# Performance work log

Hardware: AMD Instinct MI355X
Metric: run time of the kernel (lower is better)

The kernel has to match this reference:

```python
import jax, jax.numpy as jnp
import numpy as np

NF, IN_NF, N_LAYERS = 64, 196, 3
B, H, W = 1, 256, 256
P3 = [(1, 1), (1, 1)]
P1 = [(0, 0), (0, 0)]


def conv2d(x, w, pad):
    return jax.lax.conv_general_dilated(x, w, (1, 1), pad,
                                        dimension_numbers=('NCHW', 'OIHW', 'NCHW'))


def prelu(x, a):
    return jnp.where(x >= 0, x, a[None, :, None, None] * x)


def warp(x, flow):
    # standard backward bilinear warp, zero padding outside the image
    Bx, C, Hx, Wx = x.shape
    yy, xx = jnp.meshgrid(jnp.arange(Hx, dtype=x.dtype),
                          jnp.arange(Wx, dtype=x.dtype), indexing='ij')
    px = xx[None] + flow[:, 0]  # (B,H,W)
    py = yy[None] + flow[:, 1]

    def sample(img, px, py):  # img (C,H,W); px,py (H,W)
        x0 = jnp.floor(px)
        y0 = jnp.floor(py)
        x1 = x0 + 1.0
        y1 = y0 + 1.0
        wx1 = px - x0
        wx0 = 1.0 - wx1
        wy1 = py - y0
        wy0 = 1.0 - wy1

        def gather(xi, yi):
            valid = (xi >= 0) & (xi <= Wx - 1) & (yi >= 0) & (yi <= Hx - 1)
            xc = jnp.clip(xi, 0, Wx - 1).astype(jnp.int32)
            yc = jnp.clip(yi, 0, Hx - 1).astype(jnp.int32)
            return img[:, yc, xc] * valid.astype(img.dtype)

        return (gather(x0, y0) * (wx0 * wy0) + gather(x1, y0) * (wx1 * wy0)
                + gather(x0, y1) * (wx0 * wy1) + gather(x1, y1) * (wx1 * wy1))

    return jax.vmap(sample)(x, px, py)


def setup_inputs() -> dict:
    key = jax.random.key(0)
    ks = jax.random.split(key, 11)
    s = 0.05
    return {
        'feat_0': jax.random.normal(ks[0], (B, 64, H, W), jnp.float32),
        'feat_1': jax.random.normal(ks[1], (B, 64, H, W), jnp.float32),
        'feat_dense': jax.random.normal(ks[2], (B, 64, H, W), jnp.float32),
        'flow': jax.random.normal(ks[3], (B, 4, H, W), jnp.float32),
        'space_mask': jax.random.uniform(ks[4], (B, 1, H, W), jnp.float32),
        'head_w': jax.random.normal(ks[5], (IN_NF, IN_NF, 3, 3), jnp.float32) * s,
        'head_a': jnp.full((IN_NF,), 0.25, jnp.float32),
        'conv_w': jax.random.normal(ks[6], (N_LAYERS, IN_NF, IN_NF, 3, 3), jnp.float32) * s,
        'conv_a': jnp.full((N_LAYERS, IN_NF), 0.25, jnp.float32),
        'last_w': jax.random.normal(ks[7], (4 + NF, IN_NF * (N_LAYERS + 1), 1, 1), jnp.float32) * s,
        'last_b': jax.random.normal(ks[8], (4 + NF,), jnp.float32) * s,
        'mask_w': jax.random.normal(ks[9], (2, NF, 3, 3), jnp.float32) * s,
        'mask_b': jax.random.normal(ks[10], (2,), jnp.float32) * s,
    }


def reference(feat_0, feat_1, feat_dense, flow, space_mask,
              head_w, head_a, conv_w, conv_a, last_w, last_b, mask_w, mask_b):
    f0 = warp(feat_0, flow[:, :2])
    f1 = warp(feat_1, flow[:, 2:4])
    x = jnp.concatenate([f0, f1, feat_dense, flow], axis=1)  # (B, in_nf, H, W)
    sm_up = jnp.repeat(jnp.repeat(space_mask, 2, axis=2), 2, axis=3)

    # head: conv3x3 -> PReLU, then mask (dense / use_sparsity=False path)
    x = prelu(conv2d(x, head_w, P3), head_a) * space_mask
    outs = [x]
    for i in range(N_LAYERS):
        x = conv2d(x, conv_w[i], P3) * space_mask
        x = prelu(x, conv_a[i])
        outs.append(x)
    x = conv2d(jnp.concatenate(outs, axis=1), last_w, P1) + last_b[None, :, None, None]

    smn = conv2d(x[:, 4:], mask_w, P3) + mask_b[None, :, None, None]

    Bx, Cx, Hx, Wx = x.shape
    x_up = jax.image.resize(x, (Bx, Cx, 2 * Hx, 2 * Wx), method='bilinear')
    smn_up = jax.image.resize(smn, (Bx, 2, 2 * Hx, 2 * Wx), method='bilinear')

    flow_out = x_up[:, :4]
    feat_t = x_up[:, 4:]
    # eval-mode mask (training=False): hard argmax between channel 0 and 1
    mask_next = (smn_up[:, :1] > smn_up[:, 1:2]).astype(x.dtype) * sm_up
    return flow_out, feat_t, mask_next
```

## Files before the change

kernel.cpp:

```cpp
#include <hip/hip_runtime.h>

typedef _Float16 f16;
typedef _Float16 f16x8 __attribute__((ext_vector_type(8)));
typedef _Float16 f16x4 __attribute__((ext_vector_type(4)));
typedef float    f32x4 __attribute__((ext_vector_type(4)));
typedef float    f32x16 __attribute__((ext_vector_type(16)));

#define MFMA16(a,b,c) __builtin_amdgcn_mfma_f32_16x16x32_f16(a,b,c,0,0,0)
#define MFMA32(a,b,c) __builtin_amdgcn_mfma_f32_32x32x16_f16(a,b,c,0,0,0)

#define AS1 __attribute__((address_space(1)))
#define AS3 __attribute__((address_space(3)))

#define NPIX 65536
#define PXS   8
#define KHS   2064
#define K16S  4128
#define HS    8256
#define CBS   16512
#define ROWH  115584
#define RBYTES 231168
#define SBUF  ((size_t)258*RBYTES)

#define PKSUB  7168
#define PK_CONV 903168
#define NMICRO 117

#define PKL_CB  5120
#define PKL_BI  35840
#define PK1_S   3072
#define PK1_BI  39936

#define ASTG 14336

__global__ void k_pack_conv(const float* __restrict__ head_w,
                            const float* __restrict__ conv_w,
                            f16* __restrict__ dst)
{
    int t = blockIdx.x*256 + threadIdx.x;
    int lane = t & 63; t >>= 6;
    int ob  = t % 7;  t /= 7;
    int sel = t & 1;  t >>= 1;
    int kx  = t % 3;  t /= 3;
    int k16 = t & 1;  t >>= 1;
    int cb  = t % 7;  t /= 7;
    int ky  = t % 3;  t /= 3;
    int li  = t;
    if (li >= 4) return;
    if (cb == 6 && k16 == 1) return;
    const float* W = (li == 0) ? head_w : (conv_w + (size_t)(li-1)*196*196*9);
    int oc  = ob*32 + (lane & 31);
    int ic0 = cb*32 + k16*16 + (lane >> 5)*8;
    int tap = ky*3 + kx;
    f16x8 v;
#pragma unroll
    for (int j = 0; j < 8; ++j) {
        int ic = ic0 + j;
        float x = 0.f;
        if (oc < 196 && ic < 196) x = W[((size_t)oc*196 + ic)*9 + tap];
        f16 h = (f16)x;
        v[j] = (sel == 0) ? h : (f16)(x - (float)h);
    }
    int pos = ky*39 + ((cb < 6) ? (cb*6 + k16*3 + kx) : (36 + kx));
    *(f16x8*)(dst + (size_t)li*PK_CONV + (size_t)pos*PKSUB
              + (size_t)(sel*7 + ob)*512 + (size_t)lane*8) = v;
}

__global__ void k_pack_last(const float* __restrict__ last_w, f16* __restrict__ dst)
{
    int t = blockIdx.x*256 + threadIdx.x;
    if (t >= 4*7*5*2*64) return;
    int lane = t & 63; t >>= 6;
    int sel  = t & 1;  t >>= 1;
    int ob   = t % 5;  t /= 5;
    int cb   = t % 7;  t /= 7;
    int bi   = t;
    int oc = ob*16 + (lane & 15);
    int k0 = cb*32 + (lane >> 4)*8;
    f16x8 v;
#pragma unroll
    for (int j = 0; j < 8; ++j) {
        int k = k0 + j;
        float x = 0.f;
        if (oc < 68 && k < 196) x = last_w[(size_t)oc*784 + bi*196 + k];
        f16 h = (f16)x;
        v[j] = (sel == 0) ? h : (f16)(x - (float)h);
    }
    *(f16x8*)(dst + (((size_t)((bi*7+cb)*5 + ob)*2 + sel)*64 + lane)*8) = v;
}

__global__ void k_pack_last32(const float* __restrict__ last_w, f16* __restrict__ dst)
{
    int t = blockIdx.x*256 + threadIdx.x;
    if (t >= 4*13*2*3*64) return;
    int lane = t & 63; t >>= 6;
    int ob   = t % 3;  t /= 3;
    int sel  = t & 1;  t >>= 1;
    int s    = t % 13; t /= 13;
    int bi   = t;
    int cb  = (s < 12) ? (s >> 1) : 6;
    int k16 = (s < 12) ? (s & 1)  : 0;
    int oc  = ob*32 + (lane & 31);
    int ic0 = cb*32 + k16*16 + (lane >> 5)*8;
    f16x8 v;
#pragma unroll
    for (int j = 0; j < 8; ++j) {
        int ic = ic0 + j;
        float x = 0.f;
        if (oc < 68 && ic < 196) x = last_w[(size_t)oc*784 + bi*196 + ic];
        f16 h = (f16)x;
        v[j] = (sel == 0) ? h : (f16)(x - (float)h);
    }
    *(f16x8*)(dst + (size_t)bi*PK1_BI + (size_t)s*PK1_S
              + (size_t)(sel*3 + ob)*512 + (size_t)lane*8) = v;
}

__global__ void k_zero_halo(f16* __restrict__ bufA, f16* __restrict__ bufB)
{
    int c = blockIdx.x*256 + threadIdx.x;
    int end = c & 1; c >>= 1;
    int kh  = c & 1; c >>= 1;
    int k16 = c & 1; c >>= 1;
    int h   = c & 1; c >>= 1;
    int cb  = c % 7; c /= 7;
    int row = c % 258; c /= 258;
    if (c >= 2) return;
    f16* base = (c == 0) ? bufA : bufB;
    f16* p = base + (size_t)row*ROWH + cb*CBS + h*HS + k16*K16S + kh*KHS + (end ? 257 : 0)*PXS;
    f16x8 z = {(f16)0,(f16)0,(f16)0,(f16)0,(f16)0,(f16)0,(f16)0,(f16)0};
    *(f16x8*)p = z;
}

struct Gath { int o00,o01,o10,o11; float w00,w01,w10,w11; };

__device__ inline Gath mk_gath(float pxf, float pyf)
{
    float x0 = floorf(pxf), y0 = floorf(pyf);
    float x1 = x0 + 1.f, y1 = y0 + 1.f;
    float wx1 = pxf - x0, wx0 = 1.f - wx1;
    float wy1 = pyf - y0, wy0 = 1.f - wy1;
    bool vx0 = (x0 >= 0.f) && (x0 <= 255.f);
    bool vx1 = (x1 >= 0.f) && (x1 <= 255.f);
    bool vy0 = (y0 >= 0.f) && (y0 <= 255.f);
    bool vy1 = (y1 >= 0.f) && (y1 <= 255.f);
    int ix0 = min(max((int)x0, 0), 255);
    int ix1 = min(max((int)x1, 0), 255);
    int iy0 = min(max((int)y0, 0), 255);
    int iy1 = min(max((int)y1, 0), 255);
    Gath g;
    g.o00 = iy0*256 + ix0; g.w00 = (vx0 && vy0) ? wx0*wy0 : 0.f;
    g.o01 = iy0*256 + ix1; g.w01 = (vx1 && vy0) ? wx1*wy0 : 0.f;
    g.o10 = iy1*256 + ix0; g.w10 = (vx0 && vy1) ? wx0*wy1 : 0.f;
    g.o11 = iy1*256 + ix1; g.w11 = (vx1 && vy1) ? wx1*wy1 : 0.f;
    return g;
}

__device__ inline void store4n(f16* __restrict__ rowb, int slot, int c0,
                               float a, float b, float c, float d)
{
    f16x4 hi, lo;
    f16 h;
    h = (f16)a; hi[0] = h; lo[0] = (f16)(a - (float)h);
    h = (f16)b; hi[1] = h; lo[1] = (f16)(b - (float)h);
    h = (f16)c; hi[2] = h; lo[2] = (f16)(c - (float)h);
    h = (f16)d; hi[3] = h; lo[3] = (f16)(d - (float)h);
    int cb = c0 >> 5, w32 = c0 & 31;
    f16* p = rowb + cb*CBS + (w32 >> 4)*K16S + ((w32 >> 3) & 1)*KHS
                 + (size_t)slot*PXS + (w32 & 7);
    *(f16x4*)p        = hi;
    *(f16x4*)(p + HS) = lo;
}

__global__ void k_warp_concat(const float* __restrict__ f0, const float* __restrict__ f1,
                              const float* __restrict__ fd, const float* __restrict__ flow,
                              f16* __restrict__ out)
{
    int px = blockIdx.x*256 + threadIdx.x;
    int row = px >> 8, col = px & 255;
    f16* rowb = out + (size_t)(row+1)*ROWH;
    int slot = col + 1;
    Gath g0 = mk_gath((float)col + flow[px],          (float)row + flow[NPIX   + px]);
    Gath g1 = mk_gath((float)col + flow[2*NPIX + px], (float)row + flow[3*NPIX + px]);
#pragma unroll
    for (int c = 0; c < 64; c += 4) {
        float v[4];
#pragma unroll
        for (int r = 0; r < 4; ++r) {
            const float* im = f0 + (size_t)(c+r)*NPIX;
            v[r] = g0.w00*im[g0.o00] + g0.w01*im[g0.o01] + g0.w10*im[g0.o10] + g0.w11*im[g0.o11];
        }
        store4n(rowb, slot, c, v[0], v[1], v[2], v[3]);
    }
#pragma unroll
    for (int c = 0; c < 64; c += 4) {
        float v[4];
#pragma unroll
        for (int r = 0; r < 4; ++r) {
            const float* im = f1 + (size_t)(c+r)*NPIX;
            v[r] = g1.w00*im[g1.o00] + g1.w01*im[g1.o01] + g1.w10*im[g1.o10] + g1.w11*im[g1.o11];
        }
        store4n(rowb, slot, 64 + c, v[0], v[1], v[2], v[3]);
    }
#pragma unroll
    for (int c = 0; c < 64; c += 4) {
        store4n(rowb, slot, 128 + c, fd[(size_t)(c+0)*NPIX + px], fd[(size_t)(c+1)*NPIX + px],
                                     fd[(size_t)(c+2)*NPIX + px], fd[(size_t)(c+3)*NPIX + px]);
    }
    store4n(rowb, slot, 192, flow[px], flow[NPIX+px], flow[2*NPIX+px], flow[3*NPIX+px]);
#pragma unroll
    for (int c = 196; c < 224; c += 4) store4n(rowb, slot, c, 0.f, 0.f, 0.f, 0.f);
}

__global__ __launch_bounds__(256, 2)
void k_conv32(const f16* __restrict__ in, f16* __restrict__ out,
              const f16* __restrict__ pack, const float* __restrict__ alpha,
              const float* __restrict__ mask, const f16* __restrict__ pk1,
              const float* __restrict__ bias1, float* __restrict__ accp, int bi1)
{
    __shared__ __align__(16) char As[2][ASTG];

    int bid = blockIdx.x;
    int wg  = (bid & 7)*64 + (bid >> 3);
    int row  = wg >> 1;
    int half = wg & 1;
    int tid  = threadIdx.x;
    int lane = tid & 63;
    int w    = tid >> 6;
    int pxt  = half*4 + w;
    int l31 = lane & 31, lk = lane >> 5;

    f32x16 acc[7];
#pragma unroll
    for (int o = 0; o < 7; ++o)
#pragma unroll
        for (int e = 0; e < 16; ++e) acc[o][e] = 0.f;
    f32x16 acc1[3];
#pragma unroll
    for (int o = 0; o < 3; ++o)
#pragma unroll
        for (int e = 0; e < 16; ++e) acc1[o][e] = 0.f;

    auto stage = [&](int b, const f16* src) {
        __builtin_amdgcn_global_load_lds(
            (const AS1 void*)(src + (size_t)tid*8),
            (AS3 void*)(&As[b][0] + tid*16), 16, 0, 0);
        __builtin_amdgcn_global_load_lds(
            (const AS1 void*)(src + (size_t)(tid+256)*8),
            (AS3 void*)(&As[b][0] + (tid+256)*16), 16, 0, 0);
        __builtin_amdgcn_global_load_lds(
            (const AS1 void*)(src + (size_t)(tid+512)*8),
            (AS3 void*)(&As[b][0] + (tid+512)*16), 16, 0, 0);
        if (tid < 128)
            __builtin_amdgcn_global_load_lds(
                (const AS1 void*)(src + (size_t)(tid+768)*8),
                (AS3 void*)(&As[b][0] + (tid+768)*16), 16, 0, 0);
    };

    auto lB = [&](const f16* bp, f16x8& H, f16x8& L) {
        H = *(const f16x8*)bp;
        L = *(const f16x8*)(bp + HS);
    };

    const f16* bcol = in + (size_t)lk*KHS + (size_t)(pxt*32 + l31)*PXS;

    f16x8 Bh0, Bl0, Bh1, Bl1;
    stage(0, pack);
    lB(bcol + (size_t)row*ROWH, Bh0, Bl0);
    __syncthreads();

    int bsel = 0, q = 0;
    for (int ky = 0; ky < 3; ++ky) {
        const f16* brow = bcol + (size_t)(row + ky)*ROWH;
        for (int cb = 0; cb < 7; ++cb) {
            const f16* bcb = brow + cb*CBS;
            const f16* bnext = (cb < 6) ? (bcb + CBS) : (brow + ROWH);
            int nk16 = (cb == 6) ? 1 : 2;
            for (int k16 = 0; k16 < 2; ++k16) {
                if (k16 >= nk16) break;
#pragma unroll
                for (int kx = 0; kx < 3; ++kx) {
                    bool last = (q == NMICRO - 1);
                    if (!last) {
                        stage(bsel ^ 1, pack + (size_t)(q+1)*PKSUB);
                        const f16* nb;
                        if (kx < 2)                  nb = bcb + k16*K16S + (kx+1)*PXS;
                        else if (k16 == 0 && cb < 6) nb = bcb + K16S;
                        else                         nb = bnext;
                        lB(nb, Bh1, Bl1);
                    }
                    bool ctr = (ky == 1) && (kx == 1) && (bi1 >= 0);
                    f16x8 A1h[3], A1l[3];
                    if (ctr) {
                        int s = (cb < 6) ? (cb*2 + k16) : 12;
                        const f16* a1 = pk1 + (size_t)bi1*PK1_BI + (size_t)s*PK1_S
                                      + (size_t)lane*8;
#pragma unroll
                        for (int o = 0; o < 3; ++o) {
                            A1h[o] = *(const f16x8*)(a1 + o*512);
                            A1l[o] = *(const f16x8*)(a1 + (3+o)*512);
                        }
                    }
                    const char* ab = &As[bsel][0];
                    __builtin_amdgcn_s_setprio(1);
#pragma unroll
                    for (int o = 0; o < 7; ++o) {
                        f16x8 Ah = *(const f16x8*)(ab + o*1024 + lane*16);
                        f16x8 Al = *(const f16x8*)(ab + (7+o)*1024 + lane*16);
                        acc[o] = MFMA32(Ah, Bh0, acc[o]);
                        acc[o] = MFMA32(Al, Bh0, acc[o]);
                        acc[o] = MFMA32(Ah, Bl0, acc[o]);
                    }
                    if (ctr) {
#pragma unroll
                        for (int o = 0; o < 3; ++o) {
                            acc1[o] = MFMA32(A1h[o], Bh0, acc1[o]);
                            acc1[o] = MFMA32(A1l[o], Bh0, acc1[o]);
                            acc1[o] = MFMA32(A1h[o], Bl0, acc1[o]);
                        }
                    }
                    __builtin_amdgcn_s_setprio(0);
                    __syncthreads();
                    bsel ^= 1; ++q;
                    Bh0 = Bh1; Bl0 = Bl1;
                }
            }
        }
    }

    float mv = mask[row*256 + pxt*32 + l31];
    f16* orow = out + (size_t)(row+1)*ROWH + (size_t)(pxt*32 + l31 + 1)*PXS + lk*4;
#pragma unroll
    for (int o = 0; o < 7; ++o) {
#pragma unroll
        for (int qg = 0; qg < 4; ++qg) {
            int oc0 = o*32 + 8*qg + 4*lk;
            f32x4 a4 = *(const f32x4*)(alpha + min(oc0, 192));
            f16x4 hi, lo;
#pragma unroll
            for (int e = 0; e < 4; ++e) {
                float v = acc[o][qg*4 + e];
                v = (v >= 0.f ? v : a4[e]*v) * mv;
                f16 h = (f16)v;
                hi[e] = h;
                lo[e] = (f16)(v - (float)h);
            }
            f16* p = orow + o*CBS + (qg >> 1)*K16S + (qg & 1)*KHS;
            *(f16x4*)p        = hi;
            *(f16x4*)(p + HS) = lo;
        }
    }
    if (bi1 >= 0) {
        int px = row*256 + pxt*32 + l31;
        float* dst = accp + (size_t)px*72;
#pragma unroll
        for (int o = 0; o < 3; ++o) {
#pragma unroll
            for (int qg = 0; qg < 4; ++qg) {
                int oc0 = o*32 + 8*qg + 4*lk;
                if (oc0 >= 72) continue;
                f32x4 d;
#pragma unroll
                for (int e = 0; e < 4; ++e) d[e] = acc1[o][qg*4 + e];
                if (bi1 == 0) {
                    f32x4 b4;
#pragma unroll
                    for (int e = 0; e < 4; ++e) b4[e] = bias1[min(oc0 + e, 67)];
                    *(f32x4*)(dst + oc0) = d + b4;
                } else {
                    *(f32x4*)(dst + oc0) = *(const f32x4*)(dst + oc0) + d;
                }
            }
        }
    }
}

__global__ __launch_bounds__(256, 4)
void k_acc_last(const f16* __restrict__ in, const f16* __restrict__ pack,
                const float* __restrict__ bias, float* __restrict__ accp, int bi)
{
    int lane = threadIdx.x & 63;
    int wid  = (blockIdx.x << 2) | (threadIdx.x >> 6);
    int row  = wid >> 3;
    int col0 = (wid & 7) << 5;
    int l15 = lane & 15, lk = lane >> 4;

    f32x4 acc[5][2];
#pragma unroll
    for (int i = 0; i < 5; ++i)
#pragma unroll
        for (int j = 0; j < 2; ++j)
            acc[i][j] = (f32x4){0.f, 0.f, 0.f, 0.f};

    const f16* bb = in + (size_t)(row+1)*ROWH + (size_t)(col0 + l15 + 1)*PXS
                  + (lk >> 1)*K16S + (lk & 1)*KHS;
    const f16* ap = pack + (size_t)bi*PKL_BI + (size_t)lane*8;
    for (int cb = 0; cb < 7; ++cb) {
        f16x8 bh[2], bl[2];
#pragma unroll
        for (int pb = 0; pb < 2; ++pb) {
            const f16* p = bb + cb*CBS + pb*16*PXS;
            bh[pb] = *(const f16x8*)p;
            bl[pb] = *(const f16x8*)(p + HS);
        }
        const f16* a = ap + cb*PKL_CB;
#pragma unroll
        for (int ob = 0; ob < 5; ++ob) {
            f16x8 ah = *(const f16x8*)(a + ob*1024);
            f16x8 al = *(const f16x8*)(a + ob*1024 + 512);
#pragma unroll
            for (int pb = 0; pb < 2; ++pb) {
                acc[ob][pb] = MFMA16(ah, bh[pb], acc[ob][pb]);
                acc[ob][pb] = MFMA16(ah, bl[pb], acc[ob][pb]);
                acc[ob][pb] = MFMA16(al, bh[pb], acc[ob][pb]);
            }
        }
    }
#pragma unroll
    for (int ob = 0; ob < 5; ++ob) {
        int oc0 = ob*16 + lk*4;
        if (oc0 >= 72) continue;
#pragma unroll
        for (int pb = 0; pb < 2; ++pb) {
            int px = row*256 + col0 + pb*16 + l15;
            float* dst = accp + (size_t)px*72 + oc0;
            *(f32x4*)dst = *(const f32x4*)dst + acc[ob][pb];
        }
    }
}

__global__ void k_smn(const float* __restrict__ accp, const float* __restrict__ mw,
                      const float* __restrict__ mb, float* __restrict__ smn)
{
    int px = blockIdx.x*256 + threadIdx.x;
    int row = px >> 8, col = px & 255;
    float s0 = mb[0], s1 = mb[1];
    for (int ky = 0; ky < 3; ++ky) {
        int r = row + ky - 1;
        if ((unsigned)r > 255u) continue;
        for (int kx = 0; kx < 3; ++kx) {
            int c = col + kx - 1;
            if ((unsigned)c > 255u) continue;
            const float* ab = accp + ((size_t)r*256 + c)*72 + 4;
            const float* w  = mw + ky*3 + kx;
#pragma unroll
            for (int ch = 0; ch < 64; ch += 4) {
                f32x4 v = *(const f32x4*)(ab + ch);
                s0 += v[0]*w[(ch+0)*9] + v[1]*w[(ch+1)*9] + v[2]*w[(ch+2)*9] + v[3]*w[(ch+3)*9];
                s1 += v[0]*w[(64+ch+0)*9] + v[1]*w[(64+ch+1)*9] + v[2]*w[(64+ch+2)*9] + v[3]*w[(64+ch+3)*9];
            }
        }
    }
    smn[px]        = s0;
    smn[NPIX + px] = s1;
}

__global__ void k_up(const float* __restrict__ accp, const float* __restrict__ smn,
                     const float* __restrict__ sm, float* __restrict__ outp)
{
    int o = blockIdx.x*256 + threadIdx.x;
    int oy = o >> 9, ox = o & 511;
    int my = oy >> 1, mx = ox >> 1;
    int r0, r1, c0, c1; float wy0, wy1, wx0, wx1;
    if (oy & 1) { r0 = my;            r1 = min(my+1, 255); wy0 = 0.75f; wy1 = 0.25f; }
    else        { r0 = max(my-1, 0);  r1 = my;             wy0 = 0.25f; wy1 = 0.75f; }
    if (ox & 1) { c0 = mx;            c1 = min(mx+1, 255); wx0 = 0.75f; wx1 = 0.25f; }
    else        { c0 = max(mx-1, 0);  c1 = mx;             wx0 = 0.25f; wx1 = 0.75f; }
    float w00 = wy0*wx0, w01 = wy0*wx1, w10 = wy1*wx0, w11 = wy1*wx1;
    int i00 = r0*256 + c0, i01 = r0*256 + c1, i10 = r1*256 + c0, i11 = r1*256 + c1;

    const float* p00 = accp + (size_t)i00*72;
    const float* p01 = accp + (size_t)i01*72;
    const float* p10 = accp + (size_t)i10*72;
    const float* p11 = accp + (size_t)i11*72;
#pragma unroll
    for (int ch = 0; ch < 68; ch += 4) {
        f32x4 va = *(const f32x4*)(p00 + ch);
        f32x4 vb = *(const f32x4*)(p01 + ch);
        f32x4 vc = *(const f32x4*)(p10 + ch);
        f32x4 vd = *(const f32x4*)(p11 + ch);
        f32x4 v;
#pragma unroll
        for (int r = 0; r < 4; ++r)
            v[r] = w00*va[r] + w01*vb[r] + w10*vc[r] + w11*vd[r];
        outp[(size_t)(ch+0)*262144 + o] = v[0];
        outp[(size_t)(ch+1)*262144 + o] = v[1];
        outp[(size_t)(ch+2)*262144 + o] = v[2];
        outp[(size_t)(ch+3)*262144 + o] = v[3];
    }
    float s0 = w00*smn[i00] + w01*smn[i01] + w10*smn[i10] + w11*smn[i11];
    float s1 = w00*smn[NPIX+i00] + w01*smn[NPIX+i01] + w10*smn[NPIX+i10] + w11*smn[NPIX+i11];
    outp[(size_t)68*262144 + o] = (s0 > s1) ? sm[my*256 + mx] : 0.f;
}

extern "C" void kernel_launch(void* const* d_in, const int* in_sizes, int n_in,
                              void* d_out, int out_size, void* d_ws, size_t ws_size,
                              hipStream_t stream)
{
    const float* feat0  = (const float*)d_in[0];
    const float* feat1  = (const float*)d_in[1];
    const float* featd  = (const float*)d_in[2];
    const float* flow   = (const float*)d_in[3];
    const float* smask  = (const float*)d_in[4];
    const float* head_w = (const float*)d_in[5];
    const float* head_a = (const float*)d_in[6];
    const float* conv_w = (const float*)d_in[7];
    const float* conv_a = (const float*)d_in[8];
    const float* last_w = (const float*)d_in[9];
    const float* last_b = (const float*)d_in[10];
    const float* mask_w = (const float*)d_in[11];
    const float* mask_b = (const float*)d_in[12];
    float* outp = (float*)d_out;

    char* ws = (char*)d_ws;
    size_t off = 0;
    f16* bufA = (f16*)(ws + off); off += SBUF;
    f16* bufB = (f16*)(ws + off); off += SBUF;
    f16* packc = (f16*)(ws + off); off += (size_t)4*PK_CONV*2;
    f16* packl = (f16*)(ws + off); off += (size_t)4*PKL_BI*2;
    f16* pack1 = (f16*)(ws + off); off += (size_t)4*PK1_BI*2;
    float* accp = (float*)(ws + off); off += (size_t)NPIX*72*4;
    float* smn  = (float*)(ws + off); off += (size_t)2*NPIX*4;

    hipMemsetAsync(bufA, 0, RBYTES, stream);
    hipMemsetAsync((char*)bufA + (size_t)257*RBYTES, 0, RBYTES, stream);
    hipMemsetAsync(bufB, 0, RBYTES, stream);
    hipMemsetAsync((char*)bufB + (size_t)257*RBYTES, 0, RBYTES, stream);
    k_zero_halo<<<226, 256, 0, stream>>>(bufA, bufB);

    k_pack_conv<<<1764, 256, 0, stream>>>(head_w, conv_w, packc);
    k_pack_last<<<70, 256, 0, stream>>>(last_w, packl);
    k_pack_last32<<<78, 256, 0, stream>>>(last_w, pack1);
    k_warp_concat<<<256, 256, 0, stream>>>(feat0, feat1, featd, flow, bufA);

    k_conv32<<<512, 256, 0, stream>>>(bufA, bufB, packc, head_a, smask,
                                      pack1, last_b, accp, -1);
    k_conv32<<<512, 256, 0, stream>>>(bufB, bufA, packc + (size_t)1*PK_CONV, conv_a, smask,
                                      pack1, last_b, accp, 0);
    k_conv32<<<512, 256, 0, stream>>>(bufA, bufB, packc + (size_t)2*PK_CONV, conv_a + 196, smask,
                                      pack1, last_b, accp, 1);
    k_conv32<<<512, 256, 0, stream>>>(bufB, bufA, packc + (size_t)3*PK_CONV, conv_a + 392, smask,
                                      pack1, last_b, accp, 2);
    k_acc_last<<<512, 256, 0, stream>>>(bufA, packl, last_b, accp, 3);

    k_smn<<<256, 256, 0, stream>>>(accp, mask_w, mask_b, smn);
    k_up<<<1024, 256, 0, stream>>>(accp, smn, smask, outp);
}
```

Measured before the change: 745.6 us.

## Triple-buffer weight staging and prefetch A-high fragments into registers on odd waves

Grows the LDS weight staging ring from two to three buffers so each weight sub-block is staged two micro-steps ahead instead of one. Odd waves also preload the next step's high-half A fragments into registers after their MFMAs, reordering their MFMA sequence so the LDS reads overlap with barrier wait. The aim is to hide global-to-LDS latency and reduce LDS read contention between waves, at the cost of more LDS per block and more VGPRs (seven extra f16x8 values), which could lower occupancy under launch_bounds(256,2).

```diff
diff --git a/kernel.cpp b/kernel.cpp
--- a/kernel.cpp
+++ b/kernel.cpp
@@ -217,7 +217,7 @@
               const float* __restrict__ mask, const f16* __restrict__ pk1,
               const float* __restrict__ bias1, float* __restrict__ accp, int bi1)
 {
-    __shared__ __align__(16) char As[2][ASTG];
+    __shared__ __align__(16) char As[3][ASTG];
 
     int bid = blockIdx.x;
     int wg  = (bid & 7)*64 + (bid >> 3);
@@ -227,6 +227,7 @@
     int lane = tid & 63;
     int w    = tid >> 6;
     int pxt  = half*4 + w;
+    int wodd = w & 1;
     int l31 = lane & 31, lk = lane >> 5;
 
     f32x16 acc[7];
@@ -265,10 +266,18 @@
 
     f16x8 Bh0, Bl0, Bh1, Bl1;
     stage(0, pack);
+    stage(1, pack + PKSUB);
     lB(bcol + (size_t)row*ROWH, Bh0, Bl0);
     __syncthreads();
 
-    int bsel = 0, q = 0;
+    f16x8 AhR[7];
+    if (wodd) {
+#pragma unroll
+        for (int o = 0; o < 7; ++o)
+            AhR[o] = *(const f16x8*)(&As[0][0] + o*1024 + lane*16);
+    }
+
+    int acur = 0, q = 0;
     for (int ky = 0; ky < 3; ++ky) {
         const f16* brow = bcol + (size_t)(row + ky)*ROWH;
         for (int cb = 0; cb < 7; ++cb) {
@@ -280,8 +289,12 @@
 #pragma unroll
                 for (int kx = 0; kx < 3; ++kx) {
                     bool last = (q == NMICRO - 1);
+                    int anx = (acur == 2) ? 0 : (acur + 1);
+                    if (q + 2 < NMICRO) {
+                        int ast = (anx == 2) ? 0 : (anx + 1);
+                        stage(ast, pack + (size_t)(q+2)*PKSUB);
+                    }
                     if (!last) {
-                        stage(bsel ^ 1, pack + (size_t)(q+1)*PKSUB);
                         const f16* nb;
                         if (kx < 2)                  nb = bcb + k16*K16S + (kx+1)*PXS;
                         else if (k16 == 0 && cb < 6) nb = bcb + K16S;
@@ -300,15 +313,25 @@
                             A1l[o] = *(const f16x8*)(a1 + (3+o)*512);
                         }
                     }
-                    const char* ab = &As[bsel][0];
+                    const char* ab = &As[acur][0];
                     __builtin_amdgcn_s_setprio(1);
-#pragma unroll
-                    for (int o = 0; o < 7; ++o) {
-                        f16x8 Ah = *(const f16x8*)(ab + o*1024 + lane*16);
-                        f16x8 Al = *(const f16x8*)(ab + (7+o)*1024 + lane*16);
-                        acc[o] = MFMA32(Ah, Bh0, acc[o]);
-                        acc[o] = MFMA32(Al, Bh0, acc[o]);
-                        acc[o] = MFMA32(Ah, Bl0, acc[o]);
+                    if (!wodd) {
+#pragma unroll
+                        for (int o = 0; o < 7; ++o) {
+                            f16x8 Ah = *(const f16x8*)(ab + o*1024 + lane*16);
+                            f16x8 Al = *(const f16x8*)(ab + (7+o)*1024 + lane*16);
+                            acc[o] = MFMA32(Ah, Bh0, acc[o]);
+                            acc[o] = MFMA32(Al, Bh0, acc[o]);
+                            acc[o] = MFMA32(Ah, Bl0, acc[o]);
+                        }
+                    } else {
+#pragma unroll
+                        for (int o = 0; o < 7; ++o) {
+                            f16x8 Al = *(const f16x8*)(ab + (7+o)*1024 + lane*16);
+                            acc[o] = MFMA32(AhR[o], Bh0, acc[o]);
+                            acc[o] = MFMA32(AhR[o], Bl0, acc[o]);
+                            acc[o] = MFMA32(Al, Bh0, acc[o]);
+                        }
                     }
                     if (ctr) {
 #pragma unroll
@@ -319,8 +342,14 @@
                         }
                     }
                     __builtin_amdgcn_s_setprio(0);
+                    if (wodd && !last) {
+                        __builtin_amdgcn_sched_barrier(0);
+#pragma unroll
+                        for (int o = 0; o < 7; ++o)
+                            AhR[o] = *(const f16x8*)(&As[anx][0] + o*1024 + lane*16);
+                    }
                     __syncthreads();
-                    bsel ^= 1; ++q;
+                    acur = anx; ++q;
                     Bh0 = Bh1; Bl0 = Bl1;
                 }
             }
```

After: 757.4 us. Within noise of the previous version (+1.6%).
